# Performance work log

Hardware: AMD Instinct MI355X
Metric: run time of the kernel (lower is better)

The kernel has to match this reference:

```python
import jax, jax.numpy as jnp
import numpy as np

GR = 16

def _conv(x, w, b, pad):
    y = jax.lax.conv_general_dilated(x, w, (1, 1), [(pad, pad), (pad, pad)],
                                     dimension_numbers=('NCHW', 'OIHW', 'NCHW'))
    return y + b[None, :, None, None]

def _build_stencil(h, w):
    num = h * w
    a = np.zeros((num, 4, num), np.float32)
    i = np.arange(num)
    m0 = ((i + 1) % w != 0) & (i + 1 < num)
    a[i[m0], 0, i[m0]] = 1.0; a[i[m0], 0, i[m0] + 1] = -1.0
    m1 = i + w < num
    a[i[m1], 1, i[m1]] = 1.0; a[i[m1], 1, i[m1] + w] = -1.0
    m2 = ((i + 2) % w != 0) & (i + 2 < num)
    a[i[m2], 2, i[m2]] = 1.0; a[i[m2], 2, i[m2] + 2] = -1.0
    m3 = i + 2 * w < num
    a[i[m3], 3, i[m3]] = 1.0; a[i[m3], 3, i[m3] + 2 * w] = -1.0
    a[-1, 0, -1] = 1.0; a[-1, 1, -1] = 1.0; a[-1, 2, -1] = 1.0; a[-1, 3, -1] = 1.0
    return jnp.asarray(a)  # (num, 4, num)

def setup_inputs() -> dict:
    key = jax.random.key(0)
    ks = jax.random.split(key, 20)
    n, c, h, w = 4, 64, 24, 24
    s = 0.02
    inp = {
        'x': jax.random.normal(ks[0], (n, c, h, w), jnp.float32),
        'a': _build_stencil(h, w),
        'grad_w1': jax.random.normal(ks[1], (c, c, 3, 3)) * s,
        'grad_b1': jnp.zeros((c,)),
        'grad_w2': jax.random.normal(ks[2], (4 * GR, c, 3, 3)) * s,
        'grad_b2': jnp.zeros((4 * GR,)),
        'att_w1': jax.random.normal(ks[3], (c, c, 3, 3)) * s,
        'att_b1': jnp.zeros((c,)),
        'att_w2': jax.random.normal(ks[4], (4 * GR, c, 3, 3)) * s,
        'att_b2': jnp.zeros((4 * GR,)),
        'se_w1': jax.random.normal(ks[5], (c // 2, c, 1, 1)) * s,
        'se_b1': jnp.zeros((c // 2,)),
        'se_w2': jax.random.normal(ks[6], (GR, c // 2, 1, 1)) * s,
        'se_b2': jnp.zeros((GR,)),
        'gn_w': jnp.ones((GR,)),
        'gn_b': jnp.zeros((GR,)),
        'post_w': jax.random.normal(ks[7], (8 * GR, GR, 3, 3)) * s,
        'post_b': jnp.zeros((8 * GR,)),
    }
    return inp

def reference(x, a, grad_w1, grad_b1, grad_w2, grad_b2,
              att_w1, att_b1, att_w2, att_b2,
              se_w1, se_b1, se_w2, se_b2,
              gn_w, gn_b, post_w, post_b):
    n, c, h, w = x.shape
    num = h * w
    # attention branch: conv -> leaky_relu -> conv -> sigmoid
    att = jax.nn.sigmoid(_conv(jax.nn.leaky_relu(_conv(x, att_w1, att_b1, 1), 0.01), att_w2, att_b2, 1))
    # gradient branch: conv -> leaky_relu -> conv
    grad = _conv(jax.nn.leaky_relu(_conv(x, grad_w1, grad_b1, 1), 0.01), grad_w2, grad_b2, 1)
    # squeeze-excite: GAP -> 1x1 conv -> leaky -> 1x1 conv -> sigmoid
    pooled = x.mean(axis=(2, 3), keepdims=True)  # (n,c,1,1)
    se = jax.nn.sigmoid(_conv(jax.nn.leaky_relu(_conv(pooled, se_w1, se_b1, 0), 0.01), se_w2, se_b2, 0))
    # reshape per-pixel 4-tap weights: (n*GR, num, 4, 1)
    att_r = att.reshape(n * GR, 4, num, 1).transpose(0, 2, 1, 3)
    grad_r = grad.reshape(n * GR, 4, num, 1).transpose(0, 2, 1, 3)
    # densified weighted stencil operator
    A = a[None] * att_r                      # (b, num, 4, num)
    B = (grad_r * att_r)[..., 0]             # (b, num, 4)
    A = A.reshape(n * GR, num * 4, num)      # (b, 4num, num)
    B = B.reshape(n * GR, num * 4)           # (b, 4num)
    ATA = jnp.einsum('bkn,bkm->bnm', A, A)   # (b, num, num)
    ATB = jnp.einsum('bkn,bk->bn', A, B)[..., None]
    ATA = ATA + jnp.eye(num, dtype=x.dtype)[None] * 1e-12
    sol = jnp.linalg.solve(ATA, ATB)         # (b, num, 1)
    y = sol.reshape(n, GR, h, w)
    # GroupNorm(1, GR): normalize over all channels + spatial, eps=1e-5
    mu = y.mean(axis=(1, 2, 3), keepdims=True)
    var = y.var(axis=(1, 2, 3), keepdims=True)
    y = (y - mu) / jnp.sqrt(var + 1e-5)
    y = y * gn_w[None, :, None, None] + gn_b[None, :, None, None]
    y = se * y
    return _conv(y, post_w, post_b, 1)
```

## Files before the change

### kernel.cpp

```cpp
#include <hip/hip_runtime.h>
#include <math.h>

#define NUM 576
#define BSTR 50
#define CTH 512
#define CHOL_LDS_BYTES ((NUM * BSTR + CTH) * sizeof(float))

__device__ __forceinline__ float leakyf(float v) { return v > 0.f ? v : 0.01f * v; }
__device__ __forceinline__ float sigmoidf(float v) { return 1.f / (1.f + __expf(-v)); }
__device__ __forceinline__ float rdlane(float v, int l) {
  return __uint_as_float(__builtin_amdgcn_readlane(__float_as_uint(v), l));
}

__global__ __launch_bounds__(576) void conv1se_kernel(
    const float* __restrict__ x,
    const float* __restrict__ wa, const float* __restrict__ ba,
    const float* __restrict__ wg, const float* __restrict__ bg,
    const float* __restrict__ sw1, const float* __restrict__ sb1,
    const float* __restrict__ sw2, const float* __restrict__ sb2,
    float* __restrict__ outa, float* __restrict__ outg,
    float* __restrict__ sev, double* __restrict__ acc)
{
  __shared__ float sx[16 * 676];
  __shared__ float pooled[64];
  __shared__ float hid[32];
  const int co = blockIdx.x, n = blockIdx.y;
  const int tid = threadIdx.x;

  if (co == 64) {
    if (tid < 2) acc[n * 2 + tid] = 0.0;
    if (tid < 64) {
      const float4* xp4 = (const float4*)(x + (size_t)(n * 64 + tid) * 576);
      float s = 0.f;
      for (int p = 0; p < 144; ++p) {
        float4 v = xp4[p];
        s += v.x + v.y + v.z + v.w;
      }
      pooled[tid] = s * (1.f / 576.f);
    }
    __syncthreads();
    if (tid < 32) {
      float h = sb1[tid];
      for (int c = 0; c < 64; ++c) h += pooled[c] * sw1[tid * 64 + c];
      hid[tid] = leakyf(h);
    }
    __syncthreads();
    if (tid < 16) {
      float v = sb2[tid];
      for (int j = 0; j < 32; ++j) v += hid[j] * sw2[tid * 32 + j];
      sev[n * 16 + tid] = sigmoidf(v);
    }
    return;
  }

  const int py = tid / 24, px = tid - py * 24;
  const int hb0 = py * 26 + px;
  for (int i = tid; i < 16 * 676; i += 576) sx[i] = 0.f;
  float acc_a = ba[co];
  float acc_g = bg[co];
  for (int c0 = 0; c0 < 64; c0 += 16) {
    __syncthreads();
#pragma unroll
    for (int q = 0; q < 4; ++q) {
      const int p = tid + q * 576;
      const int k = p / 144;
      const int r = p - k * 144;
      const int pix = r * 4;
      const int ppy = pix / 24, ppx = pix - ppy * 24;
      const float4 v = *(const float4*)&x[(size_t)(n * 64 + c0) * 576 + p * 4];
      float* d = &sx[k * 676 + (ppy + 1) * 26 + ppx + 1];
      d[0] = v.x; d[1] = v.y; d[2] = v.z; d[3] = v.w;
    }
    __syncthreads();
#pragma unroll 4
    for (int k = 0; k < 16; ++k) {
      const float* wpa = wa + (co * 64 + c0 + k) * 9;
      const float* wpg = wg + (co * 64 + c0 + k) * 9;
      const float* sp = &sx[k * 676 + hb0];
#pragma unroll
      for (int dy = 0; dy < 3; ++dy)
#pragma unroll
        for (int dx = 0; dx < 3; ++dx) {
          const float v = sp[dy * 26 + dx];
          acc_a += v * wpa[dy * 3 + dx];
          acc_g += v * wpg[dy * 3 + dx];
        }
    }
  }
  const int o = (n * 64 + co) * 576 + tid;
  outa[o] = leakyf(acc_a);
  outg[o] = leakyf(acc_g);
}

__global__ __launch_bounds__(576) void conv2_kernel(
    const float* __restrict__ t1a, const float* __restrict__ t1g,
    const float* __restrict__ wa, const float* __restrict__ ba,
    const float* __restrict__ wg, const float* __restrict__ bg,
    float* __restrict__ att, float* __restrict__ grd)
{
  __shared__ float sx[16 * 676];
  const int co = blockIdx.x, n = blockIdx.y, br = blockIdx.z;
  const float* src = br ? t1g : t1a;
  const float* wp0 = br ? wg : wa;
  const float bias = br ? bg[co] : ba[co];
  float* dst = br ? grd : att;
  const int tid = threadIdx.x;
  const int py = tid / 24, px = tid - py * 24;
  const int hb0 = py * 26 + px;
  for (int i = tid; i < 16 * 676; i += 576) sx[i] = 0.f;
  float acc = bias;
  for (int c0 = 0; c0 < 64; c0 += 16) {
    __syncthreads();
#pragma unroll
    for (int q = 0; q < 4; ++q) {
      const int p = tid + q * 576;
      const int k = p / 144;
      const int r = p - k * 144;
      const int pix = r * 4;
      const int ppy = pix / 24, ppx = pix - ppy * 24;
      const float4 v = *(const float4*)&src[(size_t)(n * 64 + c0) * 576 + p * 4];
      float* d = &sx[k * 676 + (ppy + 1) * 26 + ppx + 1];
      d[0] = v.x; d[1] = v.y; d[2] = v.z; d[3] = v.w;
    }
    __syncthreads();
#pragma unroll 4
    for (int k = 0; k < 16; ++k) {
      const float* wp = wp0 + (co * 64 + c0 + k) * 9;
      const float* sp = &sx[k * 676 + hb0];
#pragma unroll
      for (int dy = 0; dy < 3; ++dy)
#pragma unroll
        for (int dx = 0; dx < 3; ++dx)
          acc += sp[dy * 26 + dx] * wp[dy * 3 + dx];
    }
  }
  if (br == 0) acc = sigmoidf(acc);
  dst[(n * 64 + co) * 576 + tid] = acc;
}

#define BS_LOAD(ip, L, rr, tl)                                                \
  {                                                                           \
    _Pragma("unroll")                                                         \
    for (int a = 0; a < 8; ++a)                                               \
      _Pragma("unroll")                                                       \
      for (int bb = a + 1; bb < 8; ++bb)                                      \
        L[a][bb] = S[((ip) - a) * BSTR + (bb - a)];                           \
    _Pragma("unroll")                                                         \
    for (int k = 0; k < 8; ++k) rr[k] = RD_s[(ip) - k];                       \
    _Pragma("unroll")                                                         \
    for (int k = 0; k < 8; ++k) {                                             \
      const int d = 8 + t - k;                                                \
      tl[k] = (d <= 48) ? S[((ip) - k) * BSTR + d] : 0.f;                     \
    }                                                                         \
  }

#define BS_STEP(i, L, rr, tl, ipre, Lp, rrp, tlp)                             \
  {                                                                           \
    asm volatile("s_waitcnt lgkmcnt(0)" ::: "memory");                        \
    float zz[8];                                                              \
    _Pragma("unroll")                                                         \
    for (int k = 0; k < 8; ++k) zz[k] = RHS_s[(i) - k];                       \
    const int rb = (i) - 8 - t;                                               \
    const bool bok = rb >= 0;                                                 \
    const float zbv = RHS_s[bok ? rb : 0];                                    \
    if ((ipre) >= 7) BS_LOAD(ipre, Lp, rrp, tlp);                             \
    float xx[8];                                                              \
    xx[0] = zz[0] * rr[0];                                                    \
    _Pragma("unroll")                                                         \
    for (int k = 1; k < 8; ++k) {                                             \
      float a2 = zz[k];                                                       \
      _Pragma("unroll")                                                       \
      for (int m = 0; m < 8; ++m)                                             \
        if (m < k) a2 -= L[m][k] * xx[m];                                     \
      xx[k] = a2 * rr[k];                                                     \
    }                                                                         \
    float at = 0.f;                                                           \
    _Pragma("unroll")                                                         \
    for (int k = 0; k < 8; ++k) at += tl[k] * xx[k];                          \
    float* rp = bok ? &RHS_s[rb] : &DUMW[t];                                  \
    *rp = zbv - at;                                                           \
    float xv = xx[0];                                                         \
    _Pragma("unroll")                                                         \
    for (int k = 1; k < 8; ++k) xv = (t == k) ? xx[k] : xv;                   \
    if (t < 8) XS_s[(i) - t] = xv;                                            \
  }

__global__ __launch_bounds__(CTH, 1) void chol_kernel(
    const float* __restrict__ att, const float* __restrict__ grd,
    float* __restrict__ sol, double* __restrict__ acc)
{
  extern __shared__ float S[];
  __shared__ float RHS_s[NUM];
  __shared__ float RD_s[NUM];
  __shared__ float XS_s[NUM];
  __shared__ __align__(16) float CP[2][8][64];
  __shared__ float DUMW[64];
  __shared__ double RW[16];
  const int b = blockIdx.x, tid = threadIdx.x;
  const int n = b >> 4, g = b & 15;
  const float* ac = att + (size_t)(n * 64 + g * 4) * 576;
  const float* gc = grd + (size_t)(n * 64 + g * 4) * 576;

  int r1C, r2C;
  const bool okC = tid < 90;
  {
    const int idx = okC ? tid : 0;
    int U, W;
    if (idx < 6) {
      U = (idx == 0) ? 0 : (idx < 3) ? 1 : 2;
      W = idx - U * (U + 1) / 2;
    } else {
      U = 3 + (idx - 6) / 4;
      W = (idx - 6) & 3;
    }
    r1C = 8 + 2 * U; r2C = 8 + 2 * W;
  }
  int r1N, r2N;
  const bool okN = (tid >= 64) && (tid < 64 + 210);
  {
    const int idx = okN ? (tid - 64) : 0;
    int k = (int)((sqrtf(8.f * (float)idx + 1.f) - 1.f) * 0.5f);
    while (k * (k + 1) / 2 > idx) --k;
    while ((k + 1) * (k + 2) / 2 <= idx) ++k;
    const int w = idx - k * (k + 1) / 2;
    r1N = 8 + 2 * (k + 4); r2N = 8 + 2 * (w + 4);
  }

  for (int i = tid; i < NUM * BSTR; i += CTH) S[i] = 0.f;
  __syncthreads();

  for (int i = tid; i < NUM; i += CTH) {
    float diag = 1e-12f, rv = 0.f;
    float od1 = 0.f, od2 = 0.f, od24 = 0.f, od48 = 0.f;
    if (((i + 1) % 24 != 0) && (i + 1 < NUM)) {
      float a0 = ac[0 * 576 + i]; float s = a0 * a0;
      diag += s; rv += s * gc[0 * 576 + i];
    }
    if (i - 1 >= 0 && (i % 24 != 0)) {
      float a0 = ac[0 * 576 + (i - 1)]; float s = a0 * a0;
      diag += s; rv -= s * gc[0 * 576 + (i - 1)]; od1 = -s;
    }
    if (i + 24 < NUM) {
      float a1 = ac[1 * 576 + i]; float s = a1 * a1;
      diag += s; rv += s * gc[1 * 576 + i];
    }
    if (i - 24 >= 0) {
      float a1 = ac[1 * 576 + (i - 24)]; float s = a1 * a1;
      diag += s; rv -= s * gc[1 * 576 + (i - 24)]; od24 = -s;
    }
    if (((i + 2) % 24 != 0) && (i + 2 < NUM)) {
      float a2 = ac[2 * 576 + i]; float s = a2 * a2;
      diag += s; rv += s * gc[2 * 576 + i];
    }
    if (i - 2 >= 0 && (i % 24 != 0)) {
      float a2 = ac[2 * 576 + (i - 2)]; float s = a2 * a2;
      diag += s; rv -= s * gc[2 * 576 + (i - 2)]; od2 = -s;
    }
    if (i + 48 < NUM) {
      float a3 = ac[3 * 576 + i]; float s = a3 * a3;
      diag += s; rv += s * gc[3 * 576 + i];
    }
    if (i - 48 >= 0) {
      float a3 = ac[3 * 576 + (i - 48)]; float s = a3 * a3;
      diag += s; rv -= s * gc[3 * 576 + (i - 48)]; od48 = -s;
    }
    if (i == NUM - 1) {
#pragma unroll
      for (int t = 0; t < 4; ++t) {
        float a = ac[t * 576 + (NUM - 1)]; float s = a * a;
        diag += s; rv += s * gc[t * 576 + (NUM - 1)];
      }
    }
    S[i * BSTR + 0] = diag;
    S[i * BSTR + 1] = od1;
    S[i * BSTR + 2] = od2;
    S[i * BSTR + 24] = od24;
    S[i * BSTR + 48] = od48;
    RHS_s[i] = rv;
    if (i == 0) RD_s[0] = rsqrtf(diag);
  }
  __syncthreads();

  for (int j = 0; j < NUM; j += 8) {
    const int p = (j >> 3) & 1;
    if (tid < 64) {
      const int t = tid;
      const int row = j + t;
      const bool rok = row < NUM;
      float v[8];
#pragma unroll
      for (int c = 0; c < 8; ++c) {
        const bool okc = rok && (t >= c) && (t - c <= 48);
        const int addr = okc ? (row * BSTR + (t - c)) : (NUM * BSTR + t);
        float vv = S[addr];
        v[c] = okc ? vv : 0.f;
      }
      float zb[8];
#pragma unroll
      for (int k = 0; k < 8; ++k) zb[k] = RHS_s[j + k];
      float z = RHS_s[rok ? row : j];
      z = rok ? z : 0.f;
      const float rd0 = RD_s[j];
      float rdv[8], y[8], lp[8][8];
#pragma unroll
      for (int k = 0; k < 8; ++k) {
        if (k == 0) {
          rdv[0] = rd0;
        } else {
          const float dk = rdlane(v[k], k);
          rdv[k] = rsqrtf(dk);
        }
        v[k] *= rdv[k];
#pragma unroll
        for (int m = k + 1; m < 8; ++m) {
          lp[m][k] = rdlane(v[k], m);
          v[m] -= v[k] * lp[m][k];
        }
      }
      y[0] = zb[0] * rdv[0];
#pragma unroll
      for (int k = 1; k < 8; ++k) {
        float a = zb[k];
#pragma unroll
        for (int m = 0; m < 8; ++m)
          if (m < k) a -= lp[k][m] * y[m];
        y[k] = a * rdv[k];
      }
      float zn = z;
#pragma unroll
      for (int c = 0; c < 8; ++c) zn -= v[c] * y[c];
#pragma unroll
      for (int c = 0; c < 8; ++c) {
        const bool okc = rok && (t > c) && (t - c <= 48);
        float* bp = okc ? &S[row * BSTR + (t - c)] : &S[NUM * BSTR + t];
        *bp = v[c];
        CP[p][c][t] = okc ? v[c] : 0.f;
      }
      if (t < 8) {
        float yv = y[0], rv = rdv[0];
#pragma unroll
        for (int k = 1; k < 8; ++k) {
          yv = (t == k) ? y[k] : yv;
          rv = (t == k) ? rdv[k] : rv;
        }
        RHS_s[row] = yv;
        RD_s[row] = rv;
      } else {
        float* rp = rok ? &RHS_s[row] : &DUMW[t & 63];
        *rp = zn;
      }
    } else {
      const int jp = j - 8;
      if (jp >= 0) {
        const int Rp = (NUM - 1) - jp;
        const bool a0 = okN && (r1N <= Rp);
        const bool a1 = okN && (r1N + 1 <= Rp);
        float2 cr[8], cc[8];
#pragma unroll
        for (int c = 0; c < 8; ++c) {
          cr[c] = *(const float2*)&CP[p ^ 1][c][r1N];
          cc[c] = *(const float2*)&CP[p ^ 1][c][r2N];
        }
        float s00 = 0.f, s01 = 0.f, s10 = 0.f, s11 = 0.f;
#pragma unroll
        for (int c = 0; c < 8; ++c) {
          s00 += cr[c].x * cc[c].x; s01 += cr[c].x * cc[c].y;
          s10 += cr[c].y * cc[c].x; s11 += cr[c].y * cc[c].y;
        }
        const int p00 = jp * BSTR + 51 * r1N - r2N;
        float* q00 = a0 ? &S[p00] : &S[NUM * BSTR + tid];
        float* q01 = a0 ? &S[p00 - 1] : &S[NUM * BSTR + tid];
        float* q10 = a1 ? &S[p00 + 51] : &S[NUM * BSTR + tid];
        float* q11 = a1 ? &S[p00 + 50] : &S[NUM * BSTR + tid];
        const float t00 = *q00 - s00, t01 = *q01 - s01;
        const float t10 = *q10 - s10, t11 = *q11 - s11;
        *q00 = t00; *q01 = t01; *q10 = t10; *q11 = t11;
      }
    }
    __syncthreads();
    {
      const int R = (NUM - 1) - j;
      const bool a0 = okC && (r1C <= R);
      const bool a1 = okC && (r1C + 1 <= R);
      float2 cr[8], cc[8];
#pragma unroll
      for (int c = 0; c < 8; ++c) {
        cr[c] = *(const float2*)&CP[p][c][r1C];
        cc[c] = *(const float2*)&CP[p][c][r2C];
      }
      float s00 = 0.f, s01 = 0.f, s10 = 0.f, s11 = 0.f;
#pragma unroll
      for (int c = 0; c < 8; ++c) {
        s00 += cr[c].x * cc[c].x; s01 += cr[c].x * cc[c].y;
        s10 += cr[c].y * cc[c].x; s11 += cr[c].y * cc[c].y;
      }
      const int p00 = j * BSTR + 51 * r1C - r2C;
      float* q00 = a0 ? &S[p00] : &S[NUM * BSTR + tid];
      float* q01 = a0 ? &S[p00 - 1] : &S[NUM * BSTR + tid];
      float* q10 = a1 ? &S[p00 + 51] : &S[NUM * BSTR + tid];
      float* q11 = a1 ? &S[p00 + 50] : &S[NUM * BSTR + tid];
      const float t00 = *q00 - s00, t01 = *q01 - s01;
      const float t10 = *q10 - s10, t11 = *q11 - s11;
      *q00 = t00; *q01 = t01; *q10 = t10; *q11 = t11;
      if (tid == 0 && a0)
        RD_s[j + 8] = rsqrtf(t00);
    }
    __syncthreads();
  }

  if (tid < 64) {
    const int t = tid;
    float LA[8][8], LB[8][8], rrA[8], rrB[8], tlA[8], tlB[8];
    BS_LOAD(NUM - 1, LA, rrA, tlA);
    for (int i = NUM - 1; i >= 15; i -= 16) {
      BS_STEP(i, LA, rrA, tlA, i - 8, LB, rrB, tlB);
      BS_STEP(i - 8, LB, rrB, tlB, i - 16, LA, rrA, tlA);
    }
  }
  __syncthreads();

  double ls = 0.0, ls2 = 0.0;
  for (int i = tid; i < NUM; i += CTH) {
    const float xv = XS_s[i];
    sol[(size_t)b * NUM + i] = xv;
    ls += (double)xv;
    ls2 += (double)xv * (double)xv;
  }
#pragma unroll
  for (int off = 32; off > 0; off >>= 1) {
    ls += __shfl_down(ls, off);
    ls2 += __shfl_down(ls2, off);
  }
  if ((tid & 63) == 0) {
    RW[(tid >> 6) * 2] = ls;
    RW[(tid >> 6) * 2 + 1] = ls2;
  }
  __syncthreads();
  if (tid == 0) {
    double s = 0.0, s2 = 0.0;
#pragma unroll
    for (int wv = 0; wv < 8; ++wv) { s += RW[wv * 2]; s2 += RW[wv * 2 + 1]; }
    atomicAdd(&acc[n * 2], s);
    atomicAdd(&acc[n * 2 + 1], s2);
  }
}

__global__ __launch_bounds__(576) void postgn_kernel(
    const float* __restrict__ sol, const double* __restrict__ acc,
    const float* __restrict__ sev,
    const float* __restrict__ gnw, const float* __restrict__ gnb,
    const float* __restrict__ w, const float* __restrict__ bias,
    float* __restrict__ out)
{
  __shared__ float sy[16 * 676];
  const int co = blockIdx.x, n = blockIdx.y, tid = threadIdx.x;
  const double mu_d = acc[n * 2] * (1.0 / 9216.0);
  const double var_d = acc[n * 2 + 1] * (1.0 / 9216.0) - mu_d * mu_d;
  const float rstd = (float)(1.0 / sqrt(var_d + 1e-5));
  const float muf = (float)mu_d;
  for (int i = tid; i < 16 * 676; i += 576) sy[i] = 0.f;
  __syncthreads();
#pragma unroll
  for (int q = 0; q < 4; ++q) {
    const int p = tid + q * 576;
    const int k = p / 144;
    const int r = p - k * 144;
    const int pix = r * 4;
    const int ppy = pix / 24, ppx = pix - ppy * 24;
    const float sv = sev[n * 16 + k];
    const float gw = gnw[k] * rstd;
    const float A = gw * sv;
    const float B = (gnb[k] - muf * gw) * sv;
    const float4 v = *(const float4*)&sol[(size_t)n * 9216 + p * 4];
    float* d = &sy[k * 676 + (ppy + 1) * 26 + ppx + 1];
    d[0] = v.x * A + B; d[1] = v.y * A + B;
    d[2] = v.z * A + B; d[3] = v.w * A + B;
  }
  __syncthreads();
  const int py = tid / 24, px = tid - py * 24;
  const int hb0 = py * 26 + px;
  float a = bias[co];
#pragma unroll 4
  for (int k = 0; k < 16; ++k) {
    const float* wp = w + (co * 16 + k) * 9;
    const float* sp = &sy[k * 676 + hb0];
#pragma unroll
    for (int dy = 0; dy < 3; ++dy)
#pragma unroll
      for (int dx = 0; dx < 3; ++dx)
        a += sp[dy * 26 + dx] * wp[dy * 3 + dx];
  }
  out[(size_t)(n * 128 + co) * 576 + tid] = a;
}

extern "C" void kernel_launch(void* const* d_in, const int* in_sizes, int n_in,
                              void* d_out, int out_size, void* d_ws, size_t ws_size,
                              hipStream_t stream) {
  const float* x       = (const float*)d_in[0];
  const float* grad_w1 = (const float*)d_in[2];
  const float* grad_b1 = (const float*)d_in[3];
  const float* grad_w2 = (const float*)d_in[4];
  const float* grad_b2 = (const float*)d_in[5];
  const float* att_w1  = (const float*)d_in[6];
  const float* att_b1  = (const float*)d_in[7];
  const float* att_w2  = (const float*)d_in[8];
  const float* att_b2  = (const float*)d_in[9];
  const float* se_w1   = (const float*)d_in[10];
  const float* se_b1   = (const float*)d_in[11];
  const float* se_w2   = (const float*)d_in[12];
  const float* se_b2   = (const float*)d_in[13];
  const float* gn_w    = (const float*)d_in[14];
  const float* gn_b    = (const float*)d_in[15];
  const float* post_w  = (const float*)d_in[16];
  const float* post_b  = (const float*)d_in[17];
  float* out = (float*)d_out;

  float* ws  = (float*)d_ws;
  float* t1a = ws;
  float* t1g = t1a + 147456;
  float* att = t1g + 147456;
  float* grd = att + 147456;
  float* sev = grd + 147456;
  float* sol = sev + 64;
  double* acc = (double*)(sol + 36864);

  (void)hipFuncSetAttribute((const void*)chol_kernel,
                            hipFuncAttributeMaxDynamicSharedMemorySize,
                            (int)CHOL_LDS_BYTES);

  conv1se_kernel<<<dim3(65, 4), 576, 0, stream>>>(
      x, att_w1, att_b1, grad_w1, grad_b1,
      se_w1, se_b1, se_w2, se_b2, t1a, t1g, sev, acc);
  conv2_kernel<<<dim3(64, 4, 2), 576, 0, stream>>>(t1a, t1g, att_w2, att_b2,
                                                   grad_w2, grad_b2, att, grd);
  chol_kernel<<<64, CTH, CHOL_LDS_BYTES, stream>>>(att, grd, sol, acc);
  postgn_kernel<<<dim3(128, 4), 576, 0, stream>>>(sol, acc, sev, gn_w, gn_b,
                                                  post_w, post_b, out);
}
```

Baseline: 206.3 us.

## Widen Cholesky panel to 16 columns and drop split lookahead trailing update

The banded Cholesky factorization now processes 16 columns per panel step instead of 8, which halves the number of barrier-separated iterations. The two-stage lookahead scheme is removed: near and far trailing updates are no longer split between wave 0 and the other threads with a double-buffered panel. A single unified 2x2-tile update over 300 threads replaces them, with target values preloaded before the first barrier, and the forward substitution is fused into the panel factorization loop. The trade-off is more serial register work for the panel wave and the loss of overlap between the panel and the trailing update.

```diff
diff --git a/kernel.cpp b/kernel.cpp
--- a/kernel.cpp
+++ b/kernel.cpp
@@ -193,7 +193,7 @@
   __shared__ float RHS_s[NUM];
   __shared__ float RD_s[NUM];
   __shared__ float XS_s[NUM];
-  __shared__ __align__(16) float CP[2][8][64];
+  __shared__ __align__(16) float CP[16][64];
   __shared__ float DUMW[64];
   __shared__ double RW[16];
   const int b = blockIdx.x, tid = threadIdx.x;
@@ -201,29 +201,15 @@
   const float* ac = att + (size_t)(n * 64 + g * 4) * 576;
   const float* gc = grd + (size_t)(n * 64 + g * 4) * 576;
 
-  int r1C, r2C;
-  const bool okC = tid < 90;
+  int r1A, r2A;
+  const bool okT = tid < 300;
   {
-    const int idx = okC ? tid : 0;
-    int U, W;
-    if (idx < 6) {
-      U = (idx == 0) ? 0 : (idx < 3) ? 1 : 2;
-      W = idx - U * (U + 1) / 2;
-    } else {
-      U = 3 + (idx - 6) / 4;
-      W = (idx - 6) & 3;
-    }
-    r1C = 8 + 2 * U; r2C = 8 + 2 * W;
-  }
-  int r1N, r2N;
-  const bool okN = (tid >= 64) && (tid < 64 + 210);
-  {
-    const int idx = okN ? (tid - 64) : 0;
-    int k = (int)((sqrtf(8.f * (float)idx + 1.f) - 1.f) * 0.5f);
-    while (k * (k + 1) / 2 > idx) --k;
-    while ((k + 1) * (k + 2) / 2 <= idx) ++k;
-    const int w = idx - k * (k + 1) / 2;
-    r1N = 8 + 2 * (k + 4); r2N = 8 + 2 * (w + 4);
+    const int T = okT ? tid : 0;
+    int U = (int)((sqrtf(8.f * (float)T + 1.f) - 1.f) * 0.5f);
+    while (U * (U + 1) / 2 > T) --U;
+    while ((U + 1) * (U + 2) / 2 <= T) ++U;
+    const int W = T - U * (U + 1) / 2;
+    r1A = 16 + 2 * U; r2A = 16 + 2 * W;
   }
 
   for (int i = tid; i < NUM * BSTR; i += CTH) S[i] = 0.f;
@@ -281,65 +267,64 @@
   }
   __syncthreads();
 
-  for (int j = 0; j < NUM; j += 8) {
-    const int p = (j >> 3) & 1;
+  for (int j = 0; j < NUM; j += 16) {
+    const int R = (NUM - 1) - j;
+    const bool a0 = okT && (r1A <= R);
+    const bool a1 = okT && (r1A + 1 <= R);
+    const int p00 = j * BSTR + 51 * r1A - r2A;
+    float* q00 = a0 ? &S[p00] : &S[NUM * BSTR + tid];
+    float* q01 = a0 ? &S[p00 - 1] : &S[NUM * BSTR + tid];
+    float* q10 = a1 ? &S[p00 + 51] : &S[NUM * BSTR + tid];
+    float* q11 = a1 ? &S[p00 + 50] : &S[NUM * BSTR + tid];
+    const float pv00 = *q00, pv01 = *q01, pv10 = *q10, pv11 = *q11;
     if (tid < 64) {
       const int t = tid;
       const int row = j + t;
       const bool rok = row < NUM;
-      float v[8];
-#pragma unroll
-      for (int c = 0; c < 8; ++c) {
+      float v[16];
+#pragma unroll
+      for (int c = 0; c < 16; ++c) {
         const bool okc = rok && (t >= c) && (t - c <= 48);
         const int addr = okc ? (row * BSTR + (t - c)) : (NUM * BSTR + t);
         float vv = S[addr];
         v[c] = okc ? vv : 0.f;
       }
-      float zb[8];
-#pragma unroll
-      for (int k = 0; k < 8; ++k) zb[k] = RHS_s[j + k];
+      float zb[16];
+#pragma unroll
+      for (int k = 0; k < 16; ++k) zb[k] = RHS_s[j + k];
       float z = RHS_s[rok ? row : j];
       z = rok ? z : 0.f;
-      const float rd0 = RD_s[j];
-      float rdv[8], y[8], lp[8][8];
-#pragma unroll
-      for (int k = 0; k < 8; ++k) {
+      float rdv[16], y[16], yac[16];
+#pragma unroll
+      for (int k = 0; k < 16; ++k) yac[k] = 0.f;
+#pragma unroll
+      for (int k = 0; k < 16; ++k) {
         if (k == 0) {
-          rdv[0] = rd0;
+          rdv[0] = RD_s[j];
         } else {
-          const float dk = rdlane(v[k], k);
-          rdv[k] = rsqrtf(dk);
+          rdv[k] = rsqrtf(rdlane(v[k], k));
         }
         v[k] *= rdv[k];
-#pragma unroll
-        for (int m = k + 1; m < 8; ++m) {
-          lp[m][k] = rdlane(v[k], m);
-          v[m] -= v[k] * lp[m][k];
+        y[k] = (zb[k] - yac[k]) * rdv[k];
+#pragma unroll
+        for (int m = k + 1; m < 16; ++m) {
+          const float lp = rdlane(v[k], m);
+          v[m] -= v[k] * lp;
+          yac[m] += lp * y[k];
         }
-      }
-      y[0] = zb[0] * rdv[0];
-#pragma unroll
-      for (int k = 1; k < 8; ++k) {
-        float a = zb[k];
-#pragma unroll
-        for (int m = 0; m < 8; ++m)
-          if (m < k) a -= lp[k][m] * y[m];
-        y[k] = a * rdv[k];
-      }
-      float zn = z;
-#pragma unroll
-      for (int c = 0; c < 8; ++c) zn -= v[c] * y[c];
-#pragma unroll
-      for (int c = 0; c < 8; ++c) {
+        z -= v[k] * y[k];
+      }
+#pragma unroll
+      for (int c = 0; c < 16; ++c) {
         const bool okc = rok && (t > c) && (t - c <= 48);
         float* bp = okc ? &S[row * BSTR + (t - c)] : &S[NUM * BSTR + t];
         *bp = v[c];
-        CP[p][c][t] = okc ? v[c] : 0.f;
-      }
-      if (t < 8) {
+        CP[c][t] = okc ? v[c] : 0.f;
+      }
+      if (t < 16) {
         float yv = y[0], rv = rdv[0];
 #pragma unroll
-        for (int k = 1; k < 8; ++k) {
+        for (int k = 1; k < 16; ++k) {
           yv = (t == k) ? y[k] : yv;
           rv = (t == k) ? rdv[k] : rv;
         }
@@ -347,63 +332,28 @@
         RD_s[row] = rv;
       } else {
         float* rp = rok ? &RHS_s[row] : &DUMW[t & 63];
-        *rp = zn;
-      }
-    } else {
-      const int jp = j - 8;
-      if (jp >= 0) {
-        const int Rp = (NUM - 1) - jp;
-        const bool a0 = okN && (r1N <= Rp);
-        const bool a1 = okN && (r1N + 1 <= Rp);
-        float2 cr[8], cc[8];
-#pragma unroll
-        for (int c = 0; c < 8; ++c) {
-          cr[c] = *(const float2*)&CP[p ^ 1][c][r1N];
-          cc[c] = *(const float2*)&CP[p ^ 1][c][r2N];
-        }
-        float s00 = 0.f, s01 = 0.f, s10 = 0.f, s11 = 0.f;
-#pragma unroll
-        for (int c = 0; c < 8; ++c) {
-          s00 += cr[c].x * cc[c].x; s01 += cr[c].x * cc[c].y;
-          s10 += cr[c].y * cc[c].x; s11 += cr[c].y * cc[c].y;
-        }
-        const int p00 = jp * BSTR + 51 * r1N - r2N;
-        float* q00 = a0 ? &S[p00] : &S[NUM * BSTR + tid];
-        float* q01 = a0 ? &S[p00 - 1] : &S[NUM * BSTR + tid];
-        float* q10 = a1 ? &S[p00 + 51] : &S[NUM * BSTR + tid];
-        float* q11 = a1 ? &S[p00 + 50] : &S[NUM * BSTR + tid];
-        const float t00 = *q00 - s00, t01 = *q01 - s01;
-        const float t10 = *q10 - s10, t11 = *q11 - s11;
-        *q00 = t00; *q01 = t01; *q10 = t10; *q11 = t11;
+        *rp = z;
       }
     }
     __syncthreads();
     {
-      const int R = (NUM - 1) - j;
-      const bool a0 = okC && (r1C <= R);
-      const bool a1 = okC && (r1C + 1 <= R);
-      float2 cr[8], cc[8];
-#pragma unroll
-      for (int c = 0; c < 8; ++c) {
-        cr[c] = *(const float2*)&CP[p][c][r1C];
-        cc[c] = *(const float2*)&CP[p][c][r2C];
+      float2 cr[16], cc[16];
+#pragma unroll
+      for (int c = 0; c < 16; ++c) {
+        cr[c] = *(const float2*)&CP[c][r1A];
+        cc[c] = *(const float2*)&CP[c][r2A];
       }
       float s00 = 0.f, s01 = 0.f, s10 = 0.f, s11 = 0.f;
 #pragma unroll
-      for (int c = 0; c < 8; ++c) {
+      for (int c = 0; c < 16; ++c) {
         s00 += cr[c].x * cc[c].x; s01 += cr[c].x * cc[c].y;
         s10 += cr[c].y * cc[c].x; s11 += cr[c].y * cc[c].y;
       }
-      const int p00 = j * BSTR + 51 * r1C - r2C;
-      float* q00 = a0 ? &S[p00] : &S[NUM * BSTR + tid];
-      float* q01 = a0 ? &S[p00 - 1] : &S[NUM * BSTR + tid];
-      float* q10 = a1 ? &S[p00 + 51] : &S[NUM * BSTR + tid];
-      float* q11 = a1 ? &S[p00 + 50] : &S[NUM * BSTR + tid];
-      const float t00 = *q00 - s00, t01 = *q01 - s01;
-      const float t10 = *q10 - s10, t11 = *q11 - s11;
-      *q00 = t00; *q01 = t01; *q10 = t10; *q11 = t11;
+      const float t00 = pv00 - s00;
+      *q00 = t00; *q01 = pv01 - s01;
+      *q10 = pv10 - s10; *q11 = pv11 - s11;
       if (tid == 0 && a0)
-        RD_s[j + 8] = rsqrtf(t00);
+        RD_s[j + 16] = rsqrtf(t00);
     }
     __syncthreads();
   }
```

Measured after the change: 207.9 us. Within noise of the previous version (+0.8%).
